# Kernel optimization log

Measured on AMD Instinct MI355X. Metric: run time of the kernel, lower is better.

The kernel has to match this reference:

```python
import jax, jax.numpy as jnp
import numpy as np

N, H, W = 128, 128, 128
K = 9          # 3x3 kernel points
DIL = 3        # dilation of the deformable conv


def conv2d(x, w, pad, dil):
    # x: [N,C,H,W], w: [O,I,kh,kw]
    return jax.lax.conv_general_dilated(
        x, w, (1, 1), [(pad, pad), (pad, pad)], rhs_dilation=(dil, dil),
        dimension_numbers=("NCHW", "OIHW", "NCHW"))


def _bilinear_one(img, py, px):
    # img: [C,H,W]; py, px: [K,H,W] sample coords. Zero outside borders (DCNv2 semantics).
    Hh, Ww = img.shape[1], img.shape[2]
    y0f = jnp.floor(py)
    x0f = jnp.floor(px)
    y0 = y0f.astype(jnp.int32)
    x0 = x0f.astype(jnp.int32)
    ly = (py - y0f)[None]   # [1,K,H,W]
    lx = (px - x0f)[None]

    def gather(yi, xi):
        valid = ((yi >= 0) & (yi < Hh) & (xi >= 0) & (xi < Ww)).astype(img.dtype)
        yc = jnp.clip(yi, 0, Hh - 1)
        xc = jnp.clip(xi, 0, Ww - 1)
        return img[:, yc, xc] * valid[None]   # [C,K,H,W]

    v00 = gather(y0, x0)
    v01 = gather(y0, x0 + 1)
    v10 = gather(y0 + 1, x0)
    v11 = gather(y0 + 1, x0 + 1)
    return (v00 * (1 - ly) * (1 - lx) + v01 * (1 - ly) * lx
            + v10 * ly * (1 - lx) + v11 * ly * lx)


def modulated_deform_conv(x, offset, mod, w, b):
    # x: [N,C,H,W]; offset: [N,2K,H,W] with (dy,dx) interleaved per kernel point
    # (standard DCNv2 channel layout); mod: [N,K,H,W]; w: [O,C,3,3]; b: [O]
    Np, C, Hh, Ww = x.shape
    dy = offset[:, 0::2]   # [N,K,H,W]
    dx = offset[:, 1::2]
    base_y = ((jnp.repeat(jnp.arange(3), 3) - 1) * DIL).astype(x.dtype)  # [K]
    base_x = ((jnp.tile(jnp.arange(3), 3) - 1) * DIL).astype(x.dtype)
    gy = jnp.arange(Hh, dtype=x.dtype).reshape(1, 1, Hh, 1)
    gx = jnp.arange(Ww, dtype=x.dtype).reshape(1, 1, 1, Ww)
    py = dy + base_y.reshape(1, K, 1, 1) + gy   # [N,K,H,W]
    px = dx + base_x.reshape(1, K, 1, 1) + gx
    samp = jax.vmap(_bilinear_one)(x, py, px)   # [N,C,K,H,W]
    samp = samp * mod[:, None]                  # sigmoid modulation
    out = jnp.einsum("nckij,ock->noij", samp, w.reshape(w.shape[0], C, K))
    return out + b.reshape(1, -1, 1, 1)


def setup_inputs() -> dict:
    key = jax.random.key(0)
    ks = jax.random.split(key, 12)
    f32 = jnp.float32
    return {
        "mask": jax.random.normal(ks[0], (N, 1, H, W), f32),
        "x": jax.random.normal(ks[1], (N, 8, H, W), f32),
        "w1": jax.random.normal(ks[2], (2, 9, 3, 3), f32) * 0.1,      # conv1x1_1 (3x3)
        "b1": jnp.zeros((2,), f32),
        "w_off": jax.random.normal(ks[3], (27, 2, 3, 3), f32) * 0.05,  # offset/mask conv
        "w_dcn": jax.random.normal(ks[4], (2, 2, 3, 3), f32) * 0.2,    # deform conv weight
        "b_dcn": jnp.zeros((2,), f32),
        "w2": jax.random.normal(ks[5], (2, 2, 1, 1), f32) * 0.5,       # conv1x1_2
        "b2": jnp.zeros((2,), f32),
        "fc1_w": jax.random.normal(ks[6], (2048, 2 * 64 * 64), f32) * 0.01,
        "fc1_b": jnp.zeros((2048,), f32),
        "fc2_w": jax.random.normal(ks[7], (1024, 2048), f32) * 0.02,
        "fc2_b": jnp.zeros((1024,), f32),
        "io_w": jax.random.normal(ks[8], (1, 1024), f32) * 0.01,
        "io_b": jnp.zeros((1,), f32),
    }


def reference(mask, x, w1, b1, w_off, w_dcn, b_dcn, w2, b2,
              fc1_w, fc1_b, fc2_w, fc2_b, io_w, io_b):
    z = jnp.concatenate([x, mask], axis=1)                    # [N,9,H,W]
    h = conv2d(z, w1, 1, 1) + b1.reshape(1, -1, 1, 1)          # [N,2,H,W]
    om = conv2d(h, w_off, 3, 3)                               # [N,27,H,W], bias=False
    ox, oy, mm = jnp.split(om, 3, axis=1)
    offset = jnp.concatenate([ox, oy], axis=1)                # [N,18,H,W]
    mm = jax.nn.sigmoid(mm)                                   # [N,9,H,W]
    h = modulated_deform_conv(h, offset, mm, w_dcn, b_dcn)    # [N,2,H,W]
    h = jax.nn.relu(conv2d(h, w2, 0, 1) + b2.reshape(1, -1, 1, 1))
    Np, C, Hh, Ww = h.shape                                   # adaptive max pool to 64x64
    h = h.reshape(Np, C, 64, Hh // 64, 64, Ww // 64).max(axis=(3, 5))
    h = h.reshape(Np, -1)                                     # [N, 8192]
    h = jax.nn.relu(h @ fc1_w.T + fc1_b)
    h = jax.nn.relu(h @ fc2_w.T + fc2_b)
    return jax.nn.sigmoid(h @ io_w.T + io_b)                  # [N,1]
```

## Files before the change

### kernel.cpp

```cpp
#include <hip/hip_runtime.h>
#include <math.h>

#define NB   128
#define HH   128
#define WW   128
#define HW   (HH*WW)
#define POOLD 64
#define FC1_IN  8192
#define FC1_OUT 2048
#define FC2_OUT 1024

#define H1_OFF    0
#define POOL_OFF  4194304
#define FC1_OFF   5242880
#define FC2_OFF   5505024

__global__ __launch_bounds__(256) void conv1_kernel(
    const float* __restrict__ xin, const float* __restrict__ mask,
    const float* __restrict__ w1, const float* __restrict__ b1,
    float* __restrict__ h1)
{
    __shared__ float sw[164];
    __shared__ float sh[9][10][132];

    int tid = threadIdx.x;
    int n   = blockIdx.y;
    int r0  = blockIdx.x * 8;

    if (tid < 162) sw[tid] = w1[tid];
    if (tid < 2)   sw[162 + tid] = b1[tid];

    for (int i = tid; i < 90; i += 256) {
        int c  = i / 10;
        int ry = i - c * 10;
        sh[c][ry][0]   = 0.f;
        sh[c][ry][129] = 0.f;
    }

    for (int idx = tid; idx < 2880; idx += 256) {
        int c   = idx / 320;
        int rem = idx - c * 320;
        int ry  = rem >> 5;
        int x4  = (rem & 31) << 2;
        int g   = r0 - 1 + ry;
        float4 v = make_float4(0.f, 0.f, 0.f, 0.f);
        if (g >= 0 && g < HH) {
            const float* src = (c < 8) ? (xin + ((size_t)n * 8 + c) * HW)
                                       : (mask + (size_t)n * HW);
            v = *(const float4*)(src + (size_t)g * WW + x4);
        }
        float* d = &sh[c][ry][x4 + 1];
        d[0] = v.x; d[1] = v.y; d[2] = v.z; d[3] = v.w;
    }
    __syncthreads();

    int x  = tid & 127;
    int yb = (tid >> 7) * 4;

    float acc[4][2];
    #pragma unroll
    for (int r = 0; r < 4; ++r) { acc[r][0] = sw[162]; acc[r][1] = sw[163]; }

    for (int c = 0; c < 9; ++c) {
        float v[6][3];
        #pragma unroll
        for (int iy = 0; iy < 6; ++iy)
            #pragma unroll
            for (int kx = 0; kx < 3; ++kx)
                v[iy][kx] = sh[c][yb + iy][x + kx];
        #pragma unroll
        for (int r = 0; r < 4; ++r)
            #pragma unroll
            for (int ky = 0; ky < 3; ++ky)
                #pragma unroll
                for (int kx = 0; kx < 3; ++kx) {
                    float t = v[r + ky][kx];
                    acc[r][0] += t * sw[c * 9 + ky * 3 + kx];
                    acc[r][1] += t * sw[81 + c * 9 + ky * 3 + kx];
                }
    }

    #pragma unroll
    for (int r = 0; r < 4; ++r) {
        size_t base = (size_t)n * (2 * HW) + (size_t)(r0 + yb + r) * WW + x;
        h1[base]      = acc[r][0];
        h1[base + HW] = acc[r][1];
    }
}

#define HALO_Y 5
#define HALO_X 6
#define SROWS  18
#define SCOLS  140

__device__ __forceinline__ void fetchg(
    const float* __restrict__ h0, const float* __restrict__ hb,
    int yi, int xi, float& a, float& b)
{
    a = 0.f; b = 0.f;
    if ((unsigned)yi < (unsigned)HH && (unsigned)xi < (unsigned)WW) {
        a = h0[yi * WW + xi];
        b = hb[yi * WW + xi];
    }
}

__global__ __launch_bounds__(256, 4) void fused_dcn_kernel(
    const float* __restrict__ h1,
    const float* __restrict__ w_off,
    const float* __restrict__ w_dcn,
    const float* __restrict__ b_dcn,
    const float* __restrict__ w2,
    const float* __restrict__ b2,
    float* __restrict__ pooled)
{
    __shared__ __align__(16) float sh[SROWS * SCOLS * 2];
    __shared__ float sw[530];

    int tid = threadIdx.x;
    int n   = blockIdx.y;
    int r0  = blockIdx.x * 8;

    for (int i = tid; i < 530; i += 256) {
        float v;
        if (i < 486)      v = w_off[i];
        else if (i < 522) v = w_dcn[i - 486];
        else if (i < 526) v = w2[i - 522];
        else if (i < 528) v = b_dcn[i - 526];
        else              v = b2[i - 528];
        sw[i] = v;
    }

    for (int i = tid; i < (SROWS * SCOLS * 2) / 4; i += 256)
        ((float4*)sh)[i] = make_float4(0.f, 0.f, 0.f, 0.f);
    __syncthreads();

    const float* h0 = h1 + (size_t)n * (2 * HW);
    const float* hb = h0 + HW;

    for (int idx = tid; idx < SROWS * 32; idx += 256) {
        int ry = idx >> 5;
        int x4 = (idx & 31) << 2;
        int g  = r0 - HALO_Y + ry;
        if (g >= 0 && g < HH) {
            const float4 a = *(const float4*)(h0 + (size_t)g * WW + x4);
            const float4 b = *(const float4*)(hb + (size_t)g * WW + x4);
            float* d = sh + ((size_t)ry * SCOLS + HALO_X + x4) * 2;
            ((float4*)d)[0] = make_float4(a.x, b.x, a.y, b.y);
            ((float4*)d)[1] = make_float4(a.z, b.z, a.w, b.w);
        }
    }
    __syncthreads();

    const float* WOFF = sw;
    const float* WDCN = sw + 486;
    const float* W2   = sw + 522;
    const float* BDCN = sw + 526;
    const float* B2   = sw + 528;

    int pc = tid & 63;
    int pr = blockIdx.x * 4 + (tid >> 6);

    float m0 = -1e30f, m1 = -1e30f;

    #pragma unroll 1
    for (int s = 0; s < 4; ++s) {
        int y = pr * 2 + (s >> 1);
        int x = pc * 2 + (s & 1);

        const float* tb = sh + ((size_t)(y - r0 + HALO_Y) * SCOLS + (x + HALO_X)) * 2;
        float hvx[9], hvy[9];
        #pragma unroll
        for (int t = 0; t < 9; ++t) {
            const float* p = tb + ((t / 3 - 1) * 3 * SCOLS + (t % 3 - 1) * 3) * 2;
            hvx[t] = p[0]; hvy[t] = p[1];
        }

        float acc0 = 0.f, acc1 = 0.f;
        #pragma unroll 1
        for (int k = 0; k < 9; ++k) {
            const float* wy = WOFF + (2 * k) * 18;
            const float* wx = WOFF + (2 * k + 1) * 18;
            const float* wm = WOFF + (18 + k) * 18;
            float dyv = 0.f, dxv = 0.f, mv = 0.f;
            #pragma unroll
            for (int t = 0; t < 9; ++t) {
                float ha = hvx[t], hcb = hvy[t];
                dyv += ha * wy[t] + hcb * wy[9 + t];
                dxv += ha * wx[t] + hcb * wx[9 + t];
                mv  += ha * wm[t] + hcb * wm[9 + t];
            }
            float mod = 1.f / (1.f + __expf(-mv));

            float py  = (float)(y + (k / 3 - 1) * 3) + dyv;
            float pxx = (float)(x + (k % 3 - 1) * 3) + dxv;
            float y0f = floorf(py), x0f = floorf(pxx);
            int   y0 = (int)y0f,   x0 = (int)x0f;
            float ly = py - y0f,   lx = pxx - x0f;

            float a00, b00, a01, b01, a10, b10, a11, b11;
            if (fabsf(dyv) < 2.0f && fabsf(dxv) < 3.0f) {
                const float* p = sh + ((size_t)(y0 - r0 + HALO_Y) * SCOLS
                                       + (x0 + HALO_X)) * 2;
                a00 = p[0];             b00 = p[1];
                a01 = p[2];             b01 = p[3];
                a10 = p[SCOLS * 2];     b10 = p[SCOLS * 2 + 1];
                a11 = p[SCOLS * 2 + 2]; b11 = p[SCOLS * 2 + 3];
            } else {
                fetchg(h0, hb, y0,     x0,     a00, b00);
                fetchg(h0, hb, y0,     x0 + 1, a01, b01);
                fetchg(h0, hb, y0 + 1, x0,     a10, b10);
                fetchg(h0, hb, y0 + 1, x0 + 1, a11, b11);
            }

            float w00 = (1.f - ly) * (1.f - lx);
            float w01 = (1.f - ly) * lx;
            float w10 = ly * (1.f - lx);
            float w11 = ly * lx;
            float sA = (w00 * a00 + w01 * a01 + w10 * a10 + w11 * a11) * mod;
            float sB = (w00 * b00 + w01 * b01 + w10 * b10 + w11 * b11) * mod;

            acc0 += WDCN[k]      * sA + WDCN[9 + k]  * sB;
            acc1 += WDCN[18 + k] * sA + WDCN[27 + k] * sB;
        }

        float v0 = acc0 + BDCN[0];
        float v1 = acc1 + BDCN[1];
        float u0 = fmaxf(W2[0] * v0 + W2[1] * v1 + B2[0], 0.f);
        float u1 = fmaxf(W2[2] * v0 + W2[3] * v1 + B2[1], 0.f);
        m0 = fmaxf(m0, u0);
        m1 = fmaxf(m1, u1);
    }

    size_t pb = (size_t)n * FC1_IN + (size_t)pr * POOLD + pc;
    pooled[pb]        = m0;
    pooled[pb + 4096] = m1;
}

__global__ void init_bias2_kernel(
    float* __restrict__ o1, const float* __restrict__ bb1,
    float* __restrict__ o2, const float* __restrict__ bb2)
{
    int i = blockIdx.x * blockDim.x + threadIdx.x;
    if (i < NB * FC1_OUT) o1[i] = bb1[i & (FC1_OUT - 1)];
    if (i < NB * FC2_OUT) o2[i] = bb2[i & (FC2_OUT - 1)];
}

typedef __bf16 bf16x8 __attribute__((ext_vector_type(8)));
typedef float  f32x4  __attribute__((ext_vector_type(4)));

#define LDT 40

__device__ __forceinline__ unsigned short f2bf(float f) {
    unsigned int u = __float_as_uint(f);
    return (unsigned short)((u + 0x7fffu + ((u >> 16) & 1u)) >> 16);
}

__global__ __launch_bounds__(256) void gemm_bf16_splitk(
    const float* __restrict__ A, const float* __restrict__ B,
    float* __restrict__ C, int K, int Nc, int kchunk, int relu_a)
{
    __shared__ __align__(16) unsigned short As[128 * LDT];
    __shared__ __align__(16) unsigned short Bs[64 * LDT];

    int tid = threadIdx.x;
    int jt  = blockIdx.x;
    int k0  = blockIdx.y * kchunk;
    int iters = kchunk >> 5;

    int t8  = tid >> 3;
    int c16 = (tid & 7) << 2;

    const float* Ag = A + (size_t)t8 * K + k0 + c16;
    const float* Bg = B + (size_t)(jt * 64 + t8) * K + k0 + c16;

    float4 pa[4]; float4 pb[2];
    #pragma unroll
    for (int p = 0; p < 4; ++p) pa[p] = *(const float4*)(Ag + (size_t)(p * 32) * K);
    #pragma unroll
    for (int p = 0; p < 2; ++p) pb[p] = *(const float4*)(Bg + (size_t)(p * 32) * K);

    int lane = tid & 63;
    int w    = tid >> 6;
    int quad = lane >> 4;
    int r    = lane & 15;

    f32x4 acc[2][4];
    #pragma unroll
    for (int mt = 0; mt < 2; ++mt)
        #pragma unroll
        for (int nt = 0; nt < 4; ++nt)
            acc[mt][nt] = (f32x4){0.f, 0.f, 0.f, 0.f};

    for (int it = 0; it < iters; ++it) {
        #pragma unroll
        for (int p = 0; p < 4; ++p) {
            float4 v = pa[p];
            if (relu_a) {
                v.x = fmaxf(v.x, 0.f); v.y = fmaxf(v.y, 0.f);
                v.z = fmaxf(v.z, 0.f); v.w = fmaxf(v.w, 0.f);
            }
            ushort4 s = make_ushort4(f2bf(v.x), f2bf(v.y), f2bf(v.z), f2bf(v.w));
            *(ushort4*)&As[(t8 + p * 32) * LDT + c16] = s;
        }
        #pragma unroll
        for (int p = 0; p < 2; ++p) {
            float4 v = pb[p];
            ushort4 s = make_ushort4(f2bf(v.x), f2bf(v.y), f2bf(v.z), f2bf(v.w));
            *(ushort4*)&Bs[(t8 + p * 32) * LDT + c16] = s;
        }
        __syncthreads();

        if (it + 1 < iters) {
            Ag += 32; Bg += 32;
            #pragma unroll
            for (int p = 0; p < 4; ++p) pa[p] = *(const float4*)(Ag + (size_t)(p * 32) * K);
            #pragma unroll
            for (int p = 0; p < 2; ++p) pb[p] = *(const float4*)(Bg + (size_t)(p * 32) * K);
        }

        bf16x8 af[2];
        #pragma unroll
        for (int mt = 0; mt < 2; ++mt)
            af[mt] = *(const bf16x8*)&As[(w * 32 + mt * 16 + r) * LDT + quad * 8];
        bf16x8 bfr[4];
        #pragma unroll
        for (int nt = 0; nt < 4; ++nt)
            bfr[nt] = *(const bf16x8*)&Bs[(nt * 16 + r) * LDT + quad * 8];

        #pragma unroll
        for (int mt = 0; mt < 2; ++mt)
            #pragma unroll
            for (int nt = 0; nt < 4; ++nt)
                acc[mt][nt] = __builtin_amdgcn_mfma_f32_16x16x32_bf16(
                    af[mt], bfr[nt], acc[mt][nt], 0, 0, 0);

        __syncthreads();
    }

    #pragma unroll
    for (int mt = 0; mt < 2; ++mt) {
        int mrow = w * 32 + mt * 16 + quad * 4;
        #pragma unroll
        for (int nt = 0; nt < 4; ++nt) {
            int col = jt * 64 + nt * 16 + r;
            #pragma unroll
            for (int i = 0; i < 4; ++i)
                atomicAdd(C + (size_t)(mrow + i) * Nc + col, acc[mt][nt][i]);
        }
    }
}

__global__ __launch_bounds__(256) void io_kernel(
    const float* __restrict__ fc2o, const float* __restrict__ io_w,
    const float* __restrict__ io_b, float* __restrict__ out)
{
    int n = blockIdx.x;
    int tid = threadIdx.x;
    float s = 0.f;
    #pragma unroll
    for (int k = tid; k < FC2_OUT; k += 256)
        s += fmaxf(fc2o[(size_t)n * FC2_OUT + k], 0.f) * io_w[k];
    #pragma unroll
    for (int off = 32; off > 0; off >>= 1)
        s += __shfl_down(s, off, 64);
    __shared__ float red[4];
    if ((tid & 63) == 0) red[tid >> 6] = s;
    __syncthreads();
    if (tid == 0) {
        float t = red[0] + red[1] + red[2] + red[3] + io_b[0];
        out[n] = 1.f / (1.f + expf(-t));
    }
}

extern "C" void kernel_launch(void* const* d_in, const int* in_sizes, int n_in,
                              void* d_out, int out_size, void* d_ws, size_t ws_size,
                              hipStream_t stream)
{
    const float* mask  = (const float*)d_in[0];
    const float* x     = (const float*)d_in[1];
    const float* w1    = (const float*)d_in[2];
    const float* b1    = (const float*)d_in[3];
    const float* w_off = (const float*)d_in[4];
    const float* w_dcn = (const float*)d_in[5];
    const float* b_dcn = (const float*)d_in[6];
    const float* w2    = (const float*)d_in[7];
    const float* b2    = (const float*)d_in[8];
    const float* fc1_w = (const float*)d_in[9];
    const float* fc1_b = (const float*)d_in[10];
    const float* fc2_w = (const float*)d_in[11];
    const float* fc2_b = (const float*)d_in[12];
    const float* io_w  = (const float*)d_in[13];
    const float* io_b  = (const float*)d_in[14];

    float* ws      = (float*)d_ws;
    float* h1      = ws + H1_OFF;
    float* pooled  = ws + POOL_OFF;
    float* fc1_out = ws + FC1_OFF;
    float* fc2_out = ws + FC2_OFF;
    float* out     = (float*)d_out;

    conv1_kernel<<<dim3(16, NB), 256, 0, stream>>>(x, mask, w1, b1, h1);

    fused_dcn_kernel<<<dim3(16, NB), 256, 0, stream>>>(
        h1, w_off, w_dcn, b_dcn, w2, b2, pooled);

    init_bias2_kernel<<<(NB * FC1_OUT + 255) / 256, 256, 0, stream>>>(
        fc1_out, fc1_b, fc2_out, fc2_b);

    gemm_bf16_splitk<<<dim3(FC1_OUT / 64, 16), 256, 0, stream>>>(
        pooled, fc1_w, fc1_out, FC1_IN, FC1_OUT, FC1_IN / 16, 0);

    gemm_bf16_splitk<<<dim3(FC2_OUT / 64, 16), 256, 0, stream>>>(
        fc1_out, fc2_w, fc2_out, FC1_OUT, FC2_OUT, FC1_OUT / 16, 1);

    io_kernel<<<NB, 256, 0, stream>>>(fc2_out, io_w, io_b, out);
}
```

Before: 326.8 us.

## Remap DCN threads to one pixel column pair, halve tile rows, double grid

The fused DCN kernel now gives each thread two vertically adjacent pixels at consecutive x, instead of four pixels of a 2x2 pool window processed in sequence. The offset-conv weights are loaded once per kernel point and reused for both pixels. The horizontal max-pool is finished with a lane shuffle, and the tile shrinks to 4 rows, which doubles the grid to 32x128 blocks. Goals are better ILP from two independent pixel chains, coalesced x-contiguous LDS and global access, and more blocks for occupancy. The cost is more halo reloads per output (14 rows per 4, versus 18 per 8) and higher register pressure.

Measured after the change: 340.3 us. 4.1% more time.

```diff
diff --git a/kernel.cpp b/kernel.cpp
--- a/kernel.cpp
+++ b/kernel.cpp
@@ -90,7 +90,7 @@
 
 #define HALO_Y 5
 #define HALO_X 6
-#define SROWS  18
+#define SROWS  14
 #define SCOLS  140
 
 __device__ __forceinline__ void fetchg(
@@ -118,7 +118,7 @@
 
     int tid = threadIdx.x;
     int n   = blockIdx.y;
-    int r0  = blockIdx.x * 8;
+    int r0  = blockIdx.x * 4;
 
     for (int i = tid; i < 530; i += 256) {
         float v;
@@ -134,16 +134,16 @@
         ((float4*)sh)[i] = make_float4(0.f, 0.f, 0.f, 0.f);
     __syncthreads();
 
-    const float* h0 = h1 + (size_t)n * (2 * HW);
-    const float* hb = h0 + HW;
+    const float* h0g = h1 + (size_t)n * (2 * HW);
+    const float* hbg = h0g + HW;
 
     for (int idx = tid; idx < SROWS * 32; idx += 256) {
         int ry = idx >> 5;
         int x4 = (idx & 31) << 2;
         int g  = r0 - HALO_Y + ry;
         if (g >= 0 && g < HH) {
-            const float4 a = *(const float4*)(h0 + (size_t)g * WW + x4);
-            const float4 b = *(const float4*)(hb + (size_t)g * WW + x4);
+            const float4 a = *(const float4*)(h0g + (size_t)g * WW + x4);
+            const float4 b = *(const float4*)(hbg + (size_t)g * WW + x4);
             float* d = sh + ((size_t)ry * SCOLS + HALO_X + x4) * 2;
             ((float4*)d)[0] = make_float4(a.x, b.x, a.y, b.y);
             ((float4*)d)[1] = make_float4(a.z, b.z, a.w, b.w);
@@ -153,87 +153,137 @@
 
     const float* WOFF = sw;
     const float* WDCN = sw + 486;
-    const float* W2   = sw + 522;
+    const float* W2v  = sw + 522;
     const float* BDCN = sw + 526;
-    const float* B2   = sw + 528;
-
-    int pc = tid & 63;
-    int pr = blockIdx.x * 4 + (tid >> 6);
-
-    float m0 = -1e30f, m1 = -1e30f;
+    const float* B2v  = sw + 528;
+
+    int l  = tid & 63;
+    int w  = tid >> 6;
+    int xh = w & 1;
+    int rp = w >> 1;
+    int x  = l + 64 * xh;
+    int yl0 = 2 * rp;
+    int yg0 = r0 + yl0;
+
+    const float* tp0 = sh + ((size_t)(yl0 + HALO_Y) * SCOLS + (x + HALO_X)) * 2;
+    const float* tp1 = tp0 + SCOLS * 2;
+
+    float h0a[9], h0b[9], h1a[9], h1b[9];
+    #pragma unroll
+    for (int t = 0; t < 9; ++t) {
+        int off = ((t / 3 - 1) * 3 * SCOLS + (t % 3 - 1) * 3) * 2;
+        h0a[t] = tp0[off]; h0b[t] = tp0[off + 1];
+        h1a[t] = tp1[off]; h1b[t] = tp1[off + 1];
+    }
+
+    float a00 = 0.f, a01 = 0.f;
+    float a10 = 0.f, a11 = 0.f;
 
     #pragma unroll 1
-    for (int s = 0; s < 4; ++s) {
-        int y = pr * 2 + (s >> 1);
-        int x = pc * 2 + (s & 1);
-
-        const float* tb = sh + ((size_t)(y - r0 + HALO_Y) * SCOLS + (x + HALO_X)) * 2;
-        float hvx[9], hvy[9];
+    for (int k = 0; k < 9; ++k) {
+        const float* wyp = WOFF + (2 * k) * 18;
+        const float* wxp = WOFF + (2 * k + 1) * 18;
+        const float* wmp = WOFF + (18 + k) * 18;
+
+        float dy0 = 0.f, dx0 = 0.f, mv0 = 0.f;
+        float dy1 = 0.f, dx1 = 0.f, mv1 = 0.f;
         #pragma unroll
         for (int t = 0; t < 9; ++t) {
-            const float* p = tb + ((t / 3 - 1) * 3 * SCOLS + (t % 3 - 1) * 3) * 2;
-            hvx[t] = p[0]; hvy[t] = p[1];
-        }
-
-        float acc0 = 0.f, acc1 = 0.f;
-        #pragma unroll 1
-        for (int k = 0; k < 9; ++k) {
-            const float* wy = WOFF + (2 * k) * 18;
-            const float* wx = WOFF + (2 * k + 1) * 18;
-            const float* wm = WOFF + (18 + k) * 18;
-            float dyv = 0.f, dxv = 0.f, mv = 0.f;
-            #pragma unroll
-            for (int t = 0; t < 9; ++t) {
-                float ha = hvx[t], hcb = hvy[t];
-                dyv += ha * wy[t] + hcb * wy[9 + t];
-                dxv += ha * wx[t] + hcb * wx[9 + t];
-                mv  += ha * wm[t] + hcb * wm[9 + t];
+            float wyA = wyp[t], wyB = wyp[9 + t];
+            float wxA = wxp[t], wxB = wxp[9 + t];
+            float wmA = wmp[t], wmB = wmp[9 + t];
+            dy0 += h0a[t] * wyA + h0b[t] * wyB;
+            dx0 += h0a[t] * wxA + h0b[t] * wxB;
+            mv0 += h0a[t] * wmA + h0b[t] * wmB;
+            dy1 += h1a[t] * wyA + h1b[t] * wyB;
+            dx1 += h1a[t] * wxA + h1b[t] * wxB;
+            mv1 += h1a[t] * wmA + h1b[t] * wmB;
+        }
+
+        int bty = (k / 3 - 1) * 3, btx = (k % 3 - 1) * 3;
+
+        {
+            float mod = 1.f / (1.f + __expf(-mv0));
+            float py  = (float)(yg0 + bty) + dy0;
+            float px_ = (float)(x + btx) + dx0;
+            float y0f = floorf(py), x0f = floorf(px_);
+            int   y0 = (int)y0f,   x0i = (int)x0f;
+            float ly = py - y0f,   lx = px_ - x0f;
+            float A00, B00, A01, B01, A10, B10, A11, B11;
+            if (fabsf(dy0) < 2.f && fabsf(dx0) < 3.f) {
+                const float* p = sh + ((size_t)(y0 - r0 + HALO_Y) * SCOLS
+                                       + (x0i + HALO_X)) * 2;
+                A00 = p[0];             B00 = p[1];
+                A01 = p[2];             B01 = p[3];
+                A10 = p[SCOLS * 2];     B10 = p[SCOLS * 2 + 1];
+                A11 = p[SCOLS * 2 + 2]; B11 = p[SCOLS * 2 + 3];
+            } else {
+                fetchg(h0g, hbg, y0,     x0i,     A00, B00);
+                fetchg(h0g, hbg, y0,     x0i + 1, A01, B01);
+                fetchg(h0g, hbg, y0 + 1, x0i,     A10, B10);
+                fetchg(h0g, hbg, y0 + 1, x0i + 1, A11, B11);
             }
-            float mod = 1.f / (1.f + __expf(-mv));
-
-            float py  = (float)(y + (k / 3 - 1) * 3) + dyv;
-            float pxx = (float)(x + (k % 3 - 1) * 3) + dxv;
-            float y0f = floorf(py), x0f = floorf(pxx);
-            int   y0 = (int)y0f,   x0 = (int)x0f;
-            float ly = py - y0f,   lx = pxx - x0f;
-
-            float a00, b00, a01, b01, a10, b10, a11, b11;
-            if (fabsf(dyv) < 2.0f && fabsf(dxv) < 3.0f) {
-                const float* p = sh + ((size_t)(y0 - r0 + HALO_Y) * SCOLS
-                                       + (x0 + HALO_X)) * 2;
-                a00 = p[0];             b00 = p[1];
-                a01 = p[2];             b01 = p[3];
-                a10 = p[SCOLS * 2];     b10 = p[SCOLS * 2 + 1];
-                a11 = p[SCOLS * 2 + 2]; b11 = p[SCOLS * 2 + 3];
-            } else {
-                fetchg(h0, hb, y0,     x0,     a00, b00);
-                fetchg(h0, hb, y0,     x0 + 1, a01, b01);
-                fetchg(h0, hb, y0 + 1, x0,     a10, b10);
-                fetchg(h0, hb, y0 + 1, x0 + 1, a11, b11);
-            }
-
             float w00 = (1.f - ly) * (1.f - lx);
             float w01 = (1.f - ly) * lx;
             float w10 = ly * (1.f - lx);
             float w11 = ly * lx;
-            float sA = (w00 * a00 + w01 * a01 + w10 * a10 + w11 * a11) * mod;
-            float sB = (w00 * b00 + w01 * b01 + w10 * b10 + w11 * b11) * mod;
-
-            acc0 += WDCN[k]      * sA + WDCN[9 + k]  * sB;
-            acc1 += WDCN[18 + k] * sA + WDCN[27 + k] * sB;
-        }
-
-        float v0 = acc0 + BDCN[0];
-        float v1 = acc1 + BDCN[1];
-        float u0 = fmaxf(W2[0] * v0 + W2[1] * v1 + B2[0], 0.f);
-        float u1 = fmaxf(W2[2] * v0 + W2[3] * v1 + B2[1], 0.f);
-        m0 = fmaxf(m0, u0);
-        m1 = fmaxf(m1, u1);
-    }
-
-    size_t pb = (size_t)n * FC1_IN + (size_t)pr * POOLD + pc;
-    pooled[pb]        = m0;
-    pooled[pb + 4096] = m1;
+            float sA = (w00 * A00 + w01 * A01 + w10 * A10 + w11 * A11) * mod;
+            float sB = (w00 * B00 + w01 * B01 + w10 * B10 + w11 * B11) * mod;
+            a00 += WDCN[k]      * sA + WDCN[9 + k]  * sB;
+            a01 += WDCN[18 + k] * sA + WDCN[27 + k] * sB;
+        }
+
+        {
+            float mod = 1.f / (1.f + __expf(-mv1));
+            float py  = (float)(yg0 + 1 + bty) + dy1;
+            float px_ = (float)(x + btx) + dx1;
+            float y0f = floorf(py), x0f = floorf(px_);
+            int   y0 = (int)y0f,   x0i = (int)x0f;
+            float ly = py - y0f,   lx = px_ - x0f;
+            float A00, B00, A01, B01, A10, B10, A11, B11;
+            if (fabsf(dy1) < 2.f && fabsf(dx1) < 3.f) {
+                const float* p = sh + ((size_t)(y0 - r0 + HALO_Y) * SCOLS
+                                       + (x0i + HALO_X)) * 2;
+                A00 = p[0];             B00 = p[1];
+                A01 = p[2];             B01 = p[3];
+                A10 = p[SCOLS * 2];     B10 = p[SCOLS * 2 + 1];
+                A11 = p[SCOLS * 2 + 2]; B11 = p[SCOLS * 2 + 3];
+            } else {
+                fetchg(h0g, hbg, y0,     x0i,     A00, B00);
+                fetchg(h0g, hbg, y0,     x0i + 1, A01, B01);
+                fetchg(h0g, hbg, y0 + 1, x0i,     A10, B10);
+                fetchg(h0g, hbg, y0 + 1, x0i + 1, A11, B11);
+            }
+            float w00 = (1.f - ly) * (1.f - lx);
+            float w01 = (1.f - ly) * lx;
+            float w10 = ly * (1.f - lx);
+            float w11 = ly * lx;
+            float sA = (w00 * A00 + w01 * A01 + w10 * A10 + w11 * A11) * mod;
+            float sB = (w00 * B00 + w01 * B01 + w10 * B10 + w11 * B11) * mod;
+            a10 += WDCN[k]      * sA + WDCN[9 + k]  * sB;
+            a11 += WDCN[18 + k] * sA + WDCN[27 + k] * sB;
+        }
+    }
+
+    float v00 = a00 + BDCN[0], v01 = a01 + BDCN[1];
+    float u00 = fmaxf(W2v[0] * v00 + W2v[1] * v01 + B2v[0], 0.f);
+    float u01 = fmaxf(W2v[2] * v00 + W2v[3] * v01 + B2v[1], 0.f);
+    float v10 = a10 + BDCN[0], v11 = a11 + BDCN[1];
+    float u10 = fmaxf(W2v[0] * v10 + W2v[1] * v11 + B2v[0], 0.f);
+    float u11 = fmaxf(W2v[2] * v10 + W2v[3] * v11 + B2v[1], 0.f);
+    float m0 = fmaxf(u00, u10);
+    float m1 = fmaxf(u01, u11);
+
+    m0 = fmaxf(m0, __shfl_xor(m0, 1, 64));
+    m1 = fmaxf(m1, __shfl_xor(m1, 1, 64));
+
+    if ((l & 1) == 0) {
+        int pr = blockIdx.x * 2 + rp;
+        int pc = (l >> 1) + 32 * xh;
+        size_t pb = (size_t)n * FC1_IN + (size_t)pr * POOLD + pc;
+        pooled[pb]        = m0;
+        pooled[pb + 4096] = m1;
+    }
 }
 
 __global__ void init_bias2_kernel(
@@ -401,7 +451,7 @@
 
     conv1_kernel<<<dim3(16, NB), 256, 0, stream>>>(x, mask, w1, b1, h1);
 
-    fused_dcn_kernel<<<dim3(16, NB), 256, 0, stream>>>(
+    fused_dcn_kernel<<<dim3(32, NB), 256, 0, stream>>>(
         h1, w_off, w_dcn, b_dcn, w2, b2, pooled);
 
     init_bias2_kernel<<<(NB * FC1_OUT + 255) / 256, 256, 0, stream>>>(
```
